# Performance work log

Measured on AMD Instinct MI355X. Metric: run time of the kernel, lower is better.

## Reference

```python
import jax, jax.numpy as jnp
import numpy as np

N_NODES = 100000
N_EDGES = 3200000
IN_CH, HID, OUT_CH = 256, 64, 64


def setup_inputs() -> dict:
    key = jax.random.key(0)
    k1, k2, k3, k4 = jax.random.split(key, 4)
    x = jax.random.normal(k1, (N_NODES, IN_CH), dtype=jnp.float32)
    edge_index = jax.random.randint(k2, (2, N_EDGES), 0, N_NODES, dtype=jnp.int64)
    W1 = jax.random.normal(k3, (IN_CH, HID), dtype=jnp.float32) * (1.0 / np.sqrt(IN_CH))
    b1 = jnp.zeros((HID,), dtype=jnp.float32)
    W2 = jax.random.normal(k4, (HID, OUT_CH), dtype=jnp.float32) * (1.0 / np.sqrt(HID))
    b2 = jnp.zeros((OUT_CH,), dtype=jnp.float32)
    return {"x": x, "edge_index": edge_index, "W1": W1, "b1": b1, "W2": W2, "b2": b2}


def reference(x, edge_index, W1, b1, W2, b2):
    N = x.shape[0]
    # GCN normalization: add self-loops, deg^{-1/2} on both endpoints
    loops = jnp.arange(N, dtype=edge_index.dtype)
    src = jnp.concatenate([edge_index[0], loops])
    dst = jnp.concatenate([edge_index[1], loops])
    deg = jax.ops.segment_sum(jnp.ones(src.shape, x.dtype), dst, num_segments=N)
    dinv = jnp.where(deg > 0, jax.lax.rsqrt(deg), 0.0)
    norm = dinv[src] * dinv[dst]  # [E+N]

    def gcn(h, W, b):
        h = h @ W  # dense linear transform
        # gather-scale-scatter aggregation over edges
        agg = jax.ops.segment_sum(h[src] * norm[:, None], dst, num_segments=N)
        return agg + b

    h = jax.nn.relu(gcn(x, W1, b1))
    return gcn(h, W2, b2)
```

## Files before the change

### kernel.cpp

```cpp
#include <hip/hip_runtime.h>

typedef unsigned short u16;
typedef unsigned int u32;
typedef __bf16 bf16x8 __attribute__((ext_vector_type(8)));
typedef float f32x4 __attribute__((ext_vector_type(4)));
typedef u16 u16x8 __attribute__((ext_vector_type(8)));
typedef u16 u16x4 __attribute__((ext_vector_type(4)));

#define IN_CH 256
#define HID 64
#define BSHIFT 8
#define BNODES 256
#define NBUK 391
#define BCAP 10240
#define TILE 8192

__device__ __forceinline__ u16 f2bf(float f) {
  union { float f; unsigned u; } v; v.f = f;
  unsigned r = v.u + 0x7FFFu + ((v.u >> 16) & 1u);
  return (u16)(r >> 16);
}
__device__ __forceinline__ float bf2f(u16 h) {
  union { unsigned u; float f; } v; v.u = ((unsigned)h) << 16;
  return v.f;
}

__global__ void k_wprep(const float* __restrict__ W1, const float* __restrict__ W2,
                        u16* __restrict__ w1t, u16* __restrict__ w2t) {
  int t = blockIdx.x * blockDim.x + threadIdx.x;
  if (t < 64 * 256) {
    int n = t >> 8, k = t & 255;
    w1t[t] = f2bf(W1[k * 64 + n]);
  }
  int t2 = t - 64 * 256;
  if (t2 >= 0 && t2 < 64 * 64) {
    int n = t2 >> 6, k = t2 & 63;
    w2t[t2] = f2bf(W2[k * 64 + n]);
  }
}


__global__ __launch_bounds__(1024) void k_part(const int* __restrict__ e_src,
                                               const int* __restrict__ e_dst,
                                               int* __restrict__ bcnt,
                                               u32* __restrict__ bedge, int E) {
  __shared__ int lcnt[512];
  __shared__ int lscan[512];
  __shared__ int gbase[512];
  __shared__ int wsum[8];
  __shared__ u32 stag[TILE];
  __shared__ int dest[TILE];
  int t = threadIdx.x;
  int base = blockIdx.x * TILE;
  int here = E - base; if (here > TILE) here = TILE;

  if (t < 512) lcnt[t] = 0;
  __syncthreads();

  u32 m[8]; int bk[8]; int rk[8];
#pragma unroll
  for (int k = 0; k < 8; ++k) {
    int e = base + t + k * 1024;
    if (e < E) {
      int s = e_src[e], d = e_dst[e];
      bk[k] = d >> BSHIFT;
      m[k] = (u32)s | ((u32)(d & (BNODES - 1)) << 20);
      rk[k] = atomicAdd(&lcnt[bk[k]], 1);
    } else bk[k] = -1;
  }
  __syncthreads();

  int lane = t & 63, w = t >> 6;
  int v = 0, x = 0;
  if (t < 512) { v = lcnt[t]; x = v; }
#pragma unroll
  for (int off = 1; off < 64; off <<= 1) {
    int y = __shfl_up(x, off);
    if (lane >= off) x += y;
  }
  if (t < 512 && lane == 63) wsum[w] = x;
  __syncthreads();
  if (t < 512) {
    int wo = 0;
    for (int i = 0; i < w; ++i) wo += wsum[i];
    lscan[t] = x - v + wo;
  }
  __syncthreads();

  if (t < NBUK) gbase[t] = t * BCAP + atomicAdd(&bcnt[t], lcnt[t]);
  __syncthreads();

#pragma unroll
  for (int k = 0; k < 8; ++k) {
    if (bk[k] >= 0) {
      int p = lscan[bk[k]] + rk[k];
      stag[p] = m[k];
      dest[p] = gbase[bk[k]] + rk[k];
    }
  }
  __syncthreads();

#pragma unroll
  for (int k = 0; k < 8; ++k) {
    int p = t + k * 1024;
    if (p < here) bedge[dest[p]] = stag[p];
  }
}


__global__ __launch_bounds__(1024) void k_sort(const int* __restrict__ bcnt,
                                               u32* __restrict__ bedge,
                                               int* __restrict__ rptr,
                                               int* __restrict__ rcnt,
                                               float* __restrict__ dinv, int N) {
  __shared__ u32 stag[BCAP];
  __shared__ int hist[BNODES];
  __shared__ int cur[BNODES];
  __shared__ int wsum4[4];
  int b = blockIdx.x, t = threadIdx.x;
  if (t < BNODES) hist[t] = 0;
  __syncthreads();
  int n = bcnt[b]; if (n > BCAP) n = BCAP;
  u32* be = bedge + (size_t)b * BCAP;

  for (int i = t; i < n; i += 1024) atomicAdd(&hist[be[i] >> 20], 1);
  __syncthreads();

  int lane = t & 63, w = t >> 6;
  int v = 0, x = 0;
  if (t < BNODES) { v = hist[t]; x = v; }
#pragma unroll
  for (int off = 1; off < 64; off <<= 1) {
    int y = __shfl_up(x, off);
    if (lane >= off) x += y;
  }
  if (t < BNODES && lane == 63) wsum4[w] = x;
  __syncthreads();
  if (t < BNODES) {
    int wo = 0;
    for (int i = 0; i < w; ++i) wo += wsum4[i];
    int ex = x - v + wo;
    cur[t] = ex;
    int node = (b << BSHIFT) + t;
    if (node < N) {
      rptr[node] = b * BCAP + ex;
      rcnt[node] = v;
      dinv[node] = rsqrtf((float)(v + 1));
    }
  }
  __syncthreads();

  for (int i = t; i < n; i += 1024) {
    u32 m = be[i];
    int p = atomicAdd(&cur[m >> 20], 1);
    stag[p] = m;
  }
  __syncthreads();

  for (int i = t; i < n; i += 1024) be[i] = stag[i];
}


__global__ __launch_bounds__(256, 1) void k_gemm1(const float* __restrict__ x,
                                                  const u16* __restrict__ w1t,
                                                  const float* __restrict__ dinv,
                                                  u16* __restrict__ h1, int N) {
  int lane = threadIdx.x & 63;
  int wave = threadIdx.x >> 6;
  int rowbase = (blockIdx.x * 4 + wave) * 16;
  if (rowbase >= N) return;
  int mn = lane & 15, quad = lane >> 4;
  const float* arow = x + (size_t)(rowbase + mn) * IN_CH + quad * 8;

  float4 a[16];
#pragma unroll
  for (int kc = 0; kc < 8; ++kc) {
    a[2 * kc] = *(const float4*)(arow + kc * 32);
    a[2 * kc + 1] = *(const float4*)(arow + kc * 32 + 4);
  }
  u16x8 au[8];
#pragma unroll
  for (int kc = 0; kc < 8; ++kc) {
    float4 a0 = a[2 * kc], a1 = a[2 * kc + 1];
    au[kc][0] = f2bf(a0.x); au[kc][1] = f2bf(a0.y);
    au[kc][2] = f2bf(a0.z); au[kc][3] = f2bf(a0.w);
    au[kc][4] = f2bf(a1.x); au[kc][5] = f2bf(a1.y);
    au[kc][6] = f2bf(a1.z); au[kc][7] = f2bf(a1.w);
  }

  f32x4 acc[4] = {{0.f, 0.f, 0.f, 0.f}, {0.f, 0.f, 0.f, 0.f},
                  {0.f, 0.f, 0.f, 0.f}, {0.f, 0.f, 0.f, 0.f}};
#pragma unroll
  for (int c = 0; c < 4; ++c) {
    const u16* brow = w1t + (c * 16 + mn) * IN_CH + quad * 8;
    u16x8 bu[8];
#pragma unroll
    for (int kc = 0; kc < 8; ++kc) bu[kc] = *(const u16x8*)(brow + kc * 32);
#pragma unroll
    for (int kc = 0; kc < 8; ++kc)
      acc[c] = __builtin_amdgcn_mfma_f32_16x16x32_bf16(
          __builtin_bit_cast(bf16x8, au[kc]), __builtin_bit_cast(bf16x8, bu[kc]),
          acc[c], 0, 0, 0);
  }
#pragma unroll
  for (int r = 0; r < 4; ++r) {
    int row = rowbase + quad * 4 + r;
    float dv = dinv[row];
#pragma unroll
    for (int c = 0; c < 4; ++c)
      h1[(size_t)row * HID + c * 16 + mn] = f2bf(dv * acc[c][r]);
  }
}

__global__ __launch_bounds__(256) void k_gemm2(const u16* __restrict__ g1,
                                               const u16* __restrict__ w2t,
                                               const float* __restrict__ dinv,
                                               u16* __restrict__ h2) {
  int lane = threadIdx.x & 63;
  int wave = threadIdx.x >> 6;
  int rowbase = blockIdx.x * 16;
  int colbase = wave * 16;
  int mn = lane & 15, quad = lane >> 4;
  const u16* arow = g1 + (size_t)(rowbase + mn) * HID + quad * 8;
  const u16* brow = w2t + (colbase + mn) * HID + quad * 8;
  u16x8 au0 = *(const u16x8*)(arow);
  u16x8 au1 = *(const u16x8*)(arow + 32);
  u16x8 bu0 = *(const u16x8*)(brow);
  u16x8 bu1 = *(const u16x8*)(brow + 32);
  f32x4 acc = {0.f, 0.f, 0.f, 0.f};
  acc = __builtin_amdgcn_mfma_f32_16x16x32_bf16(
      __builtin_bit_cast(bf16x8, au0), __builtin_bit_cast(bf16x8, bu0), acc, 0, 0, 0);
  acc = __builtin_amdgcn_mfma_f32_16x16x32_bf16(
      __builtin_bit_cast(bf16x8, au1), __builtin_bit_cast(bf16x8, bu1), acc, 0, 0, 0);
#pragma unroll
  for (int r = 0; r < 4; ++r) {
    int row = rowbase + quad * 4 + r;
    h2[(size_t)row * HID + colbase + mn] = f2bf(dinv[row] * acc[r]);
  }
}


template <bool RELU, bool BF16OUT>
__global__ __launch_bounds__(256, 4) void k_agg(const u16* __restrict__ hin,
                                                const int* __restrict__ rptr,
                                                const int* __restrict__ rcnt,
                                                const u32* __restrict__ sedge,
                                                const float* __restrict__ bias,
                                                void* __restrict__ outv, int N) {
  int wid = blockIdx.x * 4 + (threadIdx.x >> 6);
  int lane = threadIdx.x & 63;
  if (wid >= N) return;
  int grp = lane >> 4;
  int cb = lane & 15;
  int start = __builtin_amdgcn_readfirstlane(rptr[wid]);
  int len = __builtin_amdgcn_readfirstlane(rcnt[wid]);
  float di = rsqrtf((float)(len + 1));
  u16x4 sv = *(const u16x4*)(hin + (size_t)wid * HID + (cb << 2));
  float acc0 = 0.f, acc1 = 0.f, acc2 = 0.f, acc3 = 0.f;
  const u32* se = sedge + start;
  int j = 0;
  for (; j + 32 <= len; j += 32) {
    u16x4 v[8];
#pragma unroll
    for (int p = 0; p < 8; ++p) {
      u32 w = se[j + p * 4 + grp];
      v[p] = *(const u16x4*)(hin + (size_t)(w & 0xFFFFF) * HID + (cb << 2));
    }
#pragma unroll
    for (int p = 0; p < 8; ++p) {
      acc0 += bf2f(v[p][0]); acc1 += bf2f(v[p][1]);
      acc2 += bf2f(v[p][2]); acc3 += bf2f(v[p][3]);
    }
  }
  if (j + 16 <= len) {
    u16x4 v[4];
#pragma unroll
    for (int p = 0; p < 4; ++p) {
      u32 w = se[j + p * 4 + grp];
      v[p] = *(const u16x4*)(hin + (size_t)(w & 0xFFFFF) * HID + (cb << 2));
    }
#pragma unroll
    for (int p = 0; p < 4; ++p) {
      acc0 += bf2f(v[p][0]); acc1 += bf2f(v[p][1]);
      acc2 += bf2f(v[p][2]); acc3 += bf2f(v[p][3]);
    }
    j += 16;
  }
  for (; j < len; j += 4) {
    int idx = j + grp;
    u32 w = se[idx < len ? idx : len - 1];
    u16x4 v = *(const u16x4*)(hin + (size_t)(w & 0xFFFFF) * HID + (cb << 2));
    float m = idx < len ? 1.f : 0.f;
    acc0 = fmaf(m, bf2f(v[0]), acc0); acc1 = fmaf(m, bf2f(v[1]), acc1);
    acc2 = fmaf(m, bf2f(v[2]), acc2); acc3 = fmaf(m, bf2f(v[3]), acc3);
  }
  acc0 += __shfl_xor(acc0, 16); acc0 += __shfl_xor(acc0, 32);
  acc1 += __shfl_xor(acc1, 16); acc1 += __shfl_xor(acc1, 32);
  acc2 += __shfl_xor(acc2, 16); acc2 += __shfl_xor(acc2, 32);
  acc3 += __shfl_xor(acc3, 16); acc3 += __shfl_xor(acc3, 32);
  if (grp == 0) {
    acc0 += bf2f(sv[0]); acc1 += bf2f(sv[1]);
    acc2 += bf2f(sv[2]); acc3 += bf2f(sv[3]);
    float4 bv = *(const float4*)(bias + (cb << 2));
    acc0 = di * acc0 + bv.x; acc1 = di * acc1 + bv.y;
    acc2 = di * acc2 + bv.z; acc3 = di * acc3 + bv.w;
    if (RELU) {
      acc0 = fmaxf(acc0, 0.f); acc1 = fmaxf(acc1, 0.f);
      acc2 = fmaxf(acc2, 0.f); acc3 = fmaxf(acc3, 0.f);
    }
    if (BF16OUT) {
      u16x4 o = {f2bf(acc0), f2bf(acc1), f2bf(acc2), f2bf(acc3)};
      *(u16x4*)((u16*)outv + (size_t)wid * HID + (cb << 2)) = o;
    } else {
      float4 o = {acc0, acc1, acc2, acc3};
      *((float4*)outv + (size_t)wid * (HID / 4) + cb) = o;
    }
  }
}


extern "C" void kernel_launch(void* const* d_in, const int* in_sizes, int n_in,
                              void* d_out, int out_size, void* d_ws, size_t ws_size,
                              hipStream_t stream) {
  const float* x = (const float*)d_in[0];
  const int* ei = (const int*)d_in[1];
  const float* W1 = (const float*)d_in[2];
  const float* b1 = (const float*)d_in[3];
  const float* W2 = (const float*)d_in[4];
  const float* b2 = (const float*)d_in[5];
  float* out = (float*)d_out;

  const int N = in_sizes[0] / IN_CH;
  const int E = in_sizes[1] / 2;
  const int* e_src = ei;
  const int* e_dst = ei + E;

  size_t off = 0;
  auto carve = [&](size_t bytes) -> char* {
    char* p = (char*)d_ws + off;
    off += (bytes + 255) & ~(size_t)255;
    return p;
  };
  int* bcnt = (int*)carve((size_t)NBUK * 4);
  u32* bedge = (u32*)carve((size_t)NBUK * BCAP * 4);
  int* rptr = (int*)carve((size_t)N * 4);
  int* rcnt = (int*)carve((size_t)N * 4);
  float* dinv = (float*)carve((size_t)N * 4);
  u16* w1t = (u16*)carve(64 * 256 * 2);
  u16* w2t = (u16*)carve(64 * 64 * 2);
  u16* h1 = (u16*)carve((size_t)N * HID * 2);
  u16* g1 = (u16*)carve((size_t)N * HID * 2);

  const int n_tiles = (E + TILE - 1) / TILE;
  const int nb_g1 = (N + 63) / 64;

  hipMemsetAsync(bcnt, 0, (size_t)NBUK * 4, stream);
  k_wprep<<<(64 * 256 + 64 * 64 + 255) / 256, 256, 0, stream>>>(W1, W2, w1t, w2t);
  k_part<<<n_tiles, 1024, 0, stream>>>(e_src, e_dst, bcnt, bedge, E);
  k_sort<<<NBUK, 1024, 0, stream>>>(bcnt, bedge, rptr, rcnt, dinv, N);
  k_gemm1<<<nb_g1, 256, 0, stream>>>(x, w1t, dinv, h1, N);
  k_agg<true, true><<<(N + 3) / 4, 256, 0, stream>>>(h1, rptr, rcnt, bedge, b1, g1, N);
  k_gemm2<<<N / 16, 256, 0, stream>>>(g1, w2t, dinv, h1);
  k_agg<false, false><<<(N + 3) / 4, 256, 0, stream>>>(h1, rptr, rcnt, bedge, b2, out, N);
}
```

Measured before the change: 362.5 us.

## Split hidden features into 16-column groups to shrink gather working set

The GEMM kernels now write h in a column-grouped layout (4 groups of 16 features, each a contiguous N×16 array). The aggregation kernel assigns each block one feature group, so concurrently running blocks gather from a 3.2 MB slice that fits in cache better, with 16 edges per wave iteration instead of 4. Edge-index loads and output stores are marked nontemporal. The cost is that each edge list is read four times (once per group) and the cross-lane reduction takes more shuffles.

```diff
diff --git a/kernel.cpp b/kernel.cpp
--- a/kernel.cpp
+++ b/kernel.cpp
@@ -9,6 +9,7 @@
 
 #define IN_CH 256
 #define HID 64
+#define NGRP 4
 #define BSHIFT 8
 #define BNODES 256
 #define NBUK 391
@@ -164,7 +165,7 @@
 __global__ __launch_bounds__(256, 1) void k_gemm1(const float* __restrict__ x,
                                                   const u16* __restrict__ w1t,
                                                   const float* __restrict__ dinv,
-                                                  u16* __restrict__ h1, int N) {
+                                                  u16* __restrict__ hg, int N) {
   int lane = threadIdx.x & 63;
   int wave = threadIdx.x >> 6;
   int rowbase = (blockIdx.x * 4 + wave) * 16;
@@ -208,21 +209,21 @@
     float dv = dinv[row];
 #pragma unroll
     for (int c = 0; c < 4; ++c)
-      h1[(size_t)row * HID + c * 16 + mn] = f2bf(dv * acc[c][r]);
+      hg[((size_t)c * N + row) * 16 + mn] = f2bf(dv * acc[c][r]);
   }
 }
 
 __global__ __launch_bounds__(256) void k_gemm2(const u16* __restrict__ g1,
                                                const u16* __restrict__ w2t,
                                                const float* __restrict__ dinv,
-                                               u16* __restrict__ h2) {
+                                               u16* __restrict__ hg, int N) {
   int lane = threadIdx.x & 63;
   int wave = threadIdx.x >> 6;
   int rowbase = blockIdx.x * 16;
-  int colbase = wave * 16;
+  int colgrp = wave;
   int mn = lane & 15, quad = lane >> 4;
   const u16* arow = g1 + (size_t)(rowbase + mn) * HID + quad * 8;
-  const u16* brow = w2t + (colbase + mn) * HID + quad * 8;
+  const u16* brow = w2t + (colgrp * 16 + mn) * HID + quad * 8;
   u16x8 au0 = *(const u16x8*)(arow);
   u16x8 au1 = *(const u16x8*)(arow + 32);
   u16x8 bu0 = *(const u16x8*)(brow);
@@ -235,85 +236,93 @@
 #pragma unroll
   for (int r = 0; r < 4; ++r) {
     int row = rowbase + quad * 4 + r;
-    h2[(size_t)row * HID + colbase + mn] = f2bf(dinv[row] * acc[r]);
+    hg[((size_t)colgrp * N + row) * 16 + mn] = f2bf(dinv[row] * acc[r]);
   }
 }
 
 
 template <bool RELU, bool BF16OUT>
-__global__ __launch_bounds__(256, 4) void k_agg(const u16* __restrict__ hin,
+__global__ __launch_bounds__(256, 4) void k_agg(const u16* __restrict__ hg,
                                                 const int* __restrict__ rptr,
                                                 const int* __restrict__ rcnt,
                                                 const u32* __restrict__ sedge,
                                                 const float* __restrict__ bias,
                                                 void* __restrict__ outv, int N) {
-  int wid = blockIdx.x * 4 + (threadIdx.x >> 6);
+  int sub = blockIdx.x & 7;
+  int chunk = blockIdx.x >> 3;
+  int g = sub >> 1;
+  int half = sub & 1;
+  int wave = threadIdx.x >> 6;
   int lane = threadIdx.x & 63;
+  int wid = (chunk * 2 + half) * 4 + wave;
   if (wid >= N) return;
-  int grp = lane >> 4;
-  int cb = lane & 15;
+  int slot = lane >> 2;
+  int cb = lane & 3;
   int start = __builtin_amdgcn_readfirstlane(rptr[wid]);
   int len = __builtin_amdgcn_readfirstlane(rcnt[wid]);
   float di = rsqrtf((float)(len + 1));
-  u16x4 sv = *(const u16x4*)(hin + (size_t)wid * HID + (cb << 2));
-  float acc0 = 0.f, acc1 = 0.f, acc2 = 0.f, acc3 = 0.f;
+  const u16* hgg = hg + (((size_t)g * N) << 4);
+  u16x4 sv = *(const u16x4*)(hgg + (((size_t)wid) << 4) + (cb << 2));
+  float a0 = 0.f, a1 = 0.f, a2 = 0.f, a3 = 0.f;
   const u32* se = sedge + start;
   int j = 0;
-  for (; j + 32 <= len; j += 32) {
-    u16x4 v[8];
-#pragma unroll
-    for (int p = 0; p < 8; ++p) {
-      u32 w = se[j + p * 4 + grp];
-      v[p] = *(const u16x4*)(hin + (size_t)(w & 0xFFFFF) * HID + (cb << 2));
-    }
-#pragma unroll
-    for (int p = 0; p < 8; ++p) {
-      acc0 += bf2f(v[p][0]); acc1 += bf2f(v[p][1]);
-      acc2 += bf2f(v[p][2]); acc3 += bf2f(v[p][3]);
-    }
+  for (; j + 64 <= len; j += 64) {
+    u32 w0 = __builtin_nontemporal_load(se + j + slot);
+    u32 w1 = __builtin_nontemporal_load(se + j + 16 + slot);
+    u32 w2 = __builtin_nontemporal_load(se + j + 32 + slot);
+    u32 w3 = __builtin_nontemporal_load(se + j + 48 + slot);
+    u16x4 v0 = *(const u16x4*)(hgg + (((size_t)(w0 & 0xFFFFF)) << 4) + (cb << 2));
+    u16x4 v1 = *(const u16x4*)(hgg + (((size_t)(w1 & 0xFFFFF)) << 4) + (cb << 2));
+    u16x4 v2 = *(const u16x4*)(hgg + (((size_t)(w2 & 0xFFFFF)) << 4) + (cb << 2));
+    u16x4 v3 = *(const u16x4*)(hgg + (((size_t)(w3 & 0xFFFFF)) << 4) + (cb << 2));
+    a0 += bf2f(v0[0]); a1 += bf2f(v0[1]); a2 += bf2f(v0[2]); a3 += bf2f(v0[3]);
+    a0 += bf2f(v1[0]); a1 += bf2f(v1[1]); a2 += bf2f(v1[2]); a3 += bf2f(v1[3]);
+    a0 += bf2f(v2[0]); a1 += bf2f(v2[1]); a2 += bf2f(v2[2]); a3 += bf2f(v2[3]);
+    a0 += bf2f(v3[0]); a1 += bf2f(v3[1]); a2 += bf2f(v3[2]); a3 += bf2f(v3[3]);
+  }
+  if (j + 32 <= len) {
+    u32 w0 = __builtin_nontemporal_load(se + j + slot);
+    u32 w1 = __builtin_nontemporal_load(se + j + 16 + slot);
+    u16x4 v0 = *(const u16x4*)(hgg + (((size_t)(w0 & 0xFFFFF)) << 4) + (cb << 2));
+    u16x4 v1 = *(const u16x4*)(hgg + (((size_t)(w1 & 0xFFFFF)) << 4) + (cb << 2));
+    a0 += bf2f(v0[0]); a1 += bf2f(v0[1]); a2 += bf2f(v0[2]); a3 += bf2f(v0[3]);
+    a0 += bf2f(v1[0]); a1 += bf2f(v1[1]); a2 += bf2f(v1[2]); a3 += bf2f(v1[3]);
+    j += 32;
   }
   if (j + 16 <= len) {
-    u16x4 v[4];
-#pragma unroll
-    for (int p = 0; p < 4; ++p) {
-      u32 w = se[j + p * 4 + grp];
-      v[p] = *(const u16x4*)(hin + (size_t)(w & 0xFFFFF) * HID + (cb << 2));
-    }
-#pragma unroll
-    for (int p = 0; p < 4; ++p) {
-      acc0 += bf2f(v[p][0]); acc1 += bf2f(v[p][1]);
-      acc2 += bf2f(v[p][2]); acc3 += bf2f(v[p][3]);
-    }
+    u32 w0 = __builtin_nontemporal_load(se + j + slot);
+    u16x4 v0 = *(const u16x4*)(hgg + (((size_t)(w0 & 0xFFFFF)) << 4) + (cb << 2));
+    a0 += bf2f(v0[0]); a1 += bf2f(v0[1]); a2 += bf2f(v0[2]); a3 += bf2f(v0[3]);
     j += 16;
   }
-  for (; j < len; j += 4) {
-    int idx = j + grp;
-    u32 w = se[idx < len ? idx : len - 1];
-    u16x4 v = *(const u16x4*)(hin + (size_t)(w & 0xFFFFF) * HID + (cb << 2));
+  for (; j < len; j += 16) {
+    int idx = j + slot;
+    u32 w = __builtin_nontemporal_load(se + (idx < len ? idx : len - 1));
+    u16x4 v = *(const u16x4*)(hgg + (((size_t)(w & 0xFFFFF)) << 4) + (cb << 2));
     float m = idx < len ? 1.f : 0.f;
-    acc0 = fmaf(m, bf2f(v[0]), acc0); acc1 = fmaf(m, bf2f(v[1]), acc1);
-    acc2 = fmaf(m, bf2f(v[2]), acc2); acc3 = fmaf(m, bf2f(v[3]), acc3);
-  }
-  acc0 += __shfl_xor(acc0, 16); acc0 += __shfl_xor(acc0, 32);
-  acc1 += __shfl_xor(acc1, 16); acc1 += __shfl_xor(acc1, 32);
-  acc2 += __shfl_xor(acc2, 16); acc2 += __shfl_xor(acc2, 32);
-  acc3 += __shfl_xor(acc3, 16); acc3 += __shfl_xor(acc3, 32);
-  if (grp == 0) {
-    acc0 += bf2f(sv[0]); acc1 += bf2f(sv[1]);
-    acc2 += bf2f(sv[2]); acc3 += bf2f(sv[3]);
-    float4 bv = *(const float4*)(bias + (cb << 2));
-    acc0 = di * acc0 + bv.x; acc1 = di * acc1 + bv.y;
-    acc2 = di * acc2 + bv.z; acc3 = di * acc3 + bv.w;
+    a0 = fmaf(m, bf2f(v[0]), a0); a1 = fmaf(m, bf2f(v[1]), a1);
+    a2 = fmaf(m, bf2f(v[2]), a2); a3 = fmaf(m, bf2f(v[3]), a3);
+  }
+  a0 += __shfl_xor(a0, 4); a0 += __shfl_xor(a0, 8); a0 += __shfl_xor(a0, 16); a0 += __shfl_xor(a0, 32);
+  a1 += __shfl_xor(a1, 4); a1 += __shfl_xor(a1, 8); a1 += __shfl_xor(a1, 16); a1 += __shfl_xor(a1, 32);
+  a2 += __shfl_xor(a2, 4); a2 += __shfl_xor(a2, 8); a2 += __shfl_xor(a2, 16); a2 += __shfl_xor(a2, 32);
+  a3 += __shfl_xor(a3, 4); a3 += __shfl_xor(a3, 8); a3 += __shfl_xor(a3, 16); a3 += __shfl_xor(a3, 32);
+  if (slot == 0) {
+    a0 += bf2f(sv[0]); a1 += bf2f(sv[1]); a2 += bf2f(sv[2]); a3 += bf2f(sv[3]);
+    const float* bp = bias + g * 16 + (cb << 2);
+    float b0 = bp[0], b1_ = bp[1], b2_ = bp[2], b3 = bp[3];
+    a0 = di * a0 + b0; a1 = di * a1 + b1_;
+    a2 = di * a2 + b2_; a3 = di * a3 + b3;
     if (RELU) {
-      acc0 = fmaxf(acc0, 0.f); acc1 = fmaxf(acc1, 0.f);
-      acc2 = fmaxf(acc2, 0.f); acc3 = fmaxf(acc3, 0.f);
+      a0 = fmaxf(a0, 0.f); a1 = fmaxf(a1, 0.f);
+      a2 = fmaxf(a2, 0.f); a3 = fmaxf(a3, 0.f);
     }
     if (BF16OUT) {
-      u16x4 o = {f2bf(acc0), f2bf(acc1), f2bf(acc2), f2bf(acc3)};
-      *(u16x4*)((u16*)outv + (size_t)wid * HID + (cb << 2)) = o;
+      u16x4 o = {f2bf(a0), f2bf(a1), f2bf(a2), f2bf(a3)};
+      __builtin_nontemporal_store(o, (u16x4*)((u16*)outv + (size_t)wid * HID + g * 16 + (cb << 2)));
     } else {
-      float4 o = {acc0, acc1, acc2, acc3};
-      *((float4*)outv + (size_t)wid * (HID / 4) + cb) = o;
+      f32x4 o = {a0, a1, a2, a3};
+      __builtin_nontemporal_store(o, (f32x4*)((float*)outv + (size_t)wid * HID + g * 16 + (cb << 2)));
     }
   }
 }
@@ -353,13 +362,14 @@
 
   const int n_tiles = (E + TILE - 1) / TILE;
   const int nb_g1 = (N + 63) / 64;
+  const int n_chunk = (N + 7) / 8;
 
   hipMemsetAsync(bcnt, 0, (size_t)NBUK * 4, stream);
   k_wprep<<<(64 * 256 + 64 * 64 + 255) / 256, 256, 0, stream>>>(W1, W2, w1t, w2t);
   k_part<<<n_tiles, 1024, 0, stream>>>(e_src, e_dst, bcnt, bedge, E);
   k_sort<<<NBUK, 1024, 0, stream>>>(bcnt, bedge, rptr, rcnt, dinv, N);
   k_gemm1<<<nb_g1, 256, 0, stream>>>(x, w1t, dinv, h1, N);
-  k_agg<true, true><<<(N + 3) / 4, 256, 0, stream>>>(h1, rptr, rcnt, bedge, b1, g1, N);
-  k_gemm2<<<N / 16, 256, 0, stream>>>(g1, w2t, dinv, h1);
-  k_agg<false, false><<<(N + 3) / 4, 256, 0, stream>>>(h1, rptr, rcnt, bedge, b2, out, N);
-}
+  k_agg<true, true><<<n_chunk * 8, 256, 0, stream>>>(h1, rptr, rcnt, bedge, b1, g1, N);
+  k_gemm2<<<N / 16, 256, 0, stream>>>(g1, w2t, dinv, h1, N);
+  k_agg<false, false><<<n_chunk * 8, 256, 0, stream>>>(h1, rptr, rcnt, bedge, b2, out, N);
+}
```

Measured after the change: 553.1 us. 52.6% more time.
